# Kernel tuning notes

Measured on AMD Instinct MI355X. Metric: run time of the kernel, lower is better.

Reference implementation:

```python
import jax, jax.numpy as jnp
import numpy as np

N_NODES = 50000
N_EDGES = 800000
QRY = 128
KEY = 128
VAL = 128
HEADS = 8
HEAD_FEATS = VAL // HEADS
BN_EPS = 1e-5


def setup_inputs() -> dict:
    key = jax.random.key(0)
    ks = jax.random.split(key, 12)
    inp = {
        "ft_q": jax.random.normal(ks[0], (N_NODES, QRY), dtype=jnp.float32),
        "ft_k": jax.random.normal(ks[1], (N_NODES, KEY), dtype=jnp.float32),
        "src": jax.random.randint(ks[2], (N_EDGES,), 0, N_NODES, dtype=jnp.int32),
        "dst": jax.random.randint(ks[3], (N_EDGES,), 0, N_NODES, dtype=jnp.int32),
        # learned params
        "Wq": jax.random.normal(ks[4], (VAL, QRY), dtype=jnp.float32) / np.sqrt(QRY),
        "bq": jnp.zeros((VAL,), dtype=jnp.float32),
        "Wk": jax.random.normal(ks[5], (VAL, KEY), dtype=jnp.float32) / np.sqrt(KEY),
        "Wv": jax.random.normal(ks[6], (VAL, QRY), dtype=jnp.float32) / np.sqrt(QRY),
        "attn_e": jax.random.normal(ks[7], (VAL,), dtype=jnp.float32),
        "bn_q_g": jnp.ones((QRY,), dtype=jnp.float32),
        "bn_q_b": jnp.zeros((QRY,), dtype=jnp.float32),
        "bn_k_g": jnp.ones((KEY,), dtype=jnp.float32),
        "bn_k_b": jnp.zeros((KEY,), dtype=jnp.float32),
    }
    return inp


def _batch_norm(x, gamma, beta):
    # training-mode BatchNorm1d: normalize over batch dim
    mean = jnp.mean(x, axis=0, keepdims=True)
    var = jnp.var(x, axis=0, keepdims=True)
    return (x - mean) * jax.lax.rsqrt(var + BN_EPS) * gamma + beta


def reference(ft_q, ft_k, src, dst, Wq, bq, Wk, Wv, attn_e,
              bn_q_g, bn_q_b, bn_k_g, bn_k_b):
    ft_q = _batch_norm(ft_q, bn_q_g, bn_q_b)
    ft_k = _batch_norm(ft_k, bn_k_g, bn_k_b)

    q = ft_q @ Wq.T + bq                      # [N, VAL]
    k = ft_k @ Wk.T                           # [N, VAL]
    v = (ft_q @ Wv.T).reshape(-1, HEADS, HEAD_FEATS)  # [N, H, D]

    # u_add_v: per-edge e = q[src] + k[dst]
    e = q[src] + k[dst]                       # [E, VAL]
    e = (attn_e * jax.nn.sigmoid(e)).reshape(-1, HEADS, HEAD_FEATS).sum(-1)  # [E, H]

    # edge_softmax grouped by destination node
    m = jax.ops.segment_max(e, dst, num_segments=N_NODES)   # [N, H]
    ex = jnp.exp(e - m[dst])                                # [E, H]
    s = jax.ops.segment_sum(ex, dst, num_segments=N_NODES)  # [N, H]
    a = ex / s[dst]                                         # [E, H]

    # u_mul_e_sum: scatter-sum of v[src] * a over destination
    msg = v[src] * a[:, :, None]                            # [E, H, D]
    rst = jax.ops.segment_sum(msg, dst, num_segments=N_NODES)  # [N, H, D]
    return rst.reshape(-1, VAL)
```

## Files before the change

### kernel.cpp

```cpp
#include <hip/hip_runtime.h>

#define N_NODES 50000
#define N_EDGES 800000
#define FEATS 128
#define NCHUNK 196
#define CPAD 50176
#define GEMM_BX 196
#define GEMM_BLOCKS 392
#define SCAT_BLOCKS 3125
#define NTILE 782
#define NF_WAVES 8192
#define STAT_BLOCKS 256
#define HSEG 128
#define ESEG 6250
#define HHALF 25088

typedef __attribute__((ext_vector_type(8))) short bf16x8;
typedef __attribute__((ext_vector_type(4))) float f32x4;
typedef union { uint4 u; bf16x8 v; } pack8;

__device__ __forceinline__ unsigned short f2bf(float f){
  unsigned u = __float_as_uint(f);
  u += 0x7FFF + ((u >> 16) & 1);
  return (unsigned short)(u >> 16);
}
__device__ __forceinline__ unsigned cvtpk(float lo, float hi){
  unsigned r;
  asm("v_cvt_pk_bf16_f32 %0, %1, %2" : "=v"(r) : "v"(lo), "v"(hi));
  return r;
}
__device__ __forceinline__ void unpack8(uint4 p, float* f){
  f[0]=__uint_as_float(p.x << 16); f[1]=__uint_as_float(p.x & 0xffff0000u);
  f[2]=__uint_as_float(p.y << 16); f[3]=__uint_as_float(p.y & 0xffff0000u);
  f[4]=__uint_as_float(p.z << 16); f[5]=__uint_as_float(p.z & 0xffff0000u);
  f[6]=__uint_as_float(p.w << 16); f[7]=__uint_as_float(p.w & 0xffff0000u);
}

__global__ __launch_bounds__(256) void stats_hist_kernel(
    const float* __restrict__ ftq, const float* __restrict__ ftk,
    float* __restrict__ sums, unsigned short* __restrict__ xqb,
    const int* __restrict__ dstE, unsigned short* __restrict__ rankE,
    unsigned short* __restrict__ hmat){
  __shared__ float red[4*FEATS];
  __shared__ unsigned lh[HHALF/2];
  int tid = threadIdx.x, bid = blockIdx.x;
  if (bid < STAT_BLOCKS){
    for (int i = tid; i < 4*FEATS; i += 256) red[i] = 0.f;
    __syncthreads();
    int sub = tid >> 5, c4 = tid & 31;
    const float* Xs = (sub < 4) ? ftq : ftk;
    int so = (sub < 4) ? 0 : 2*FEATS;
    bool isq = (sub < 4);
    float a0=0,a1=0,a2=0,a3=0,b0=0,b1=0,b2=0,b3=0;
    #pragma unroll 4
    for (int r = bid*4 + (sub&3); r < N_NODES; r += STAT_BLOCKS*4){
      float4 x = *(const float4*)(Xs + (size_t)r*FEATS + c4*4);
      if (isq)
        *(uint2*)&xqb[(size_t)r*FEATS + c4*4] = make_uint2(cvtpk(x.x,x.y), cvtpk(x.z,x.w));
      a0+=x.x; b0+=x.x*x.x; a1+=x.y; b1+=x.y*x.y;
      a2+=x.z; b2+=x.z*x.z; a3+=x.w; b3+=x.w*x.w;
    }
    a0 += __shfl_xor(a0,32); a1 += __shfl_xor(a1,32);
    a2 += __shfl_xor(a2,32); a3 += __shfl_xor(a3,32);
    b0 += __shfl_xor(b0,32); b1 += __shfl_xor(b1,32);
    b2 += __shfl_xor(b2,32); b3 += __shfl_xor(b3,32);
    if ((tid & 63) < 32){
      int c0 = c4*4;
      atomicAdd(&red[so + c0+0], a0); atomicAdd(&red[so + c0+1], a1);
      atomicAdd(&red[so + c0+2], a2); atomicAdd(&red[so + c0+3], a3);
      atomicAdd(&red[so + FEATS + c0+0], b0); atomicAdd(&red[so + FEATS + c0+1], b1);
      atomicAdd(&red[so + FEATS + c0+2], b2); atomicAdd(&red[so + FEATS + c0+3], b3);
    }
    __syncthreads();
    for (int i = tid; i < 4*FEATS; i += 256) atomicAdd(&sums[i], red[i]);
  } else {
    int hb = bid - STAT_BLOCKS;
    int seg = hb >> 1, hi = hb & 1;
    int dlo = hi * HHALF;
    for (int i = tid; i < HHALF/2; i += 256) lh[i] = 0;
    __syncthreads();
    int e0 = seg * ESEG;
    for (int t = e0 + tid; t < e0 + ESEG; t += 256){
      int d = dstE[t] - dlo;
      if ((unsigned)d < (unsigned)HHALF){
        unsigned sh = (d & 1) * 16;
        unsigned old = atomicAdd(&lh[d >> 1], 1u << sh);
        rankE[t] = (unsigned short)((old >> sh) & 0xffffu);
      }
    }
    __syncthreads();
    unsigned* row = (unsigned*)(hmat + (size_t)hb * HHALF);
    for (int i = tid; i < HHALF/2; i += 256) row[i] = lh[i];
  }
}

__global__ __launch_bounds__(256) void colscan_fold_kernel(
    const unsigned short* __restrict__ hmat, unsigned short* __restrict__ hbase,
    int* __restrict__ loc, int* __restrict__ csums,
    const float* __restrict__ Wq, const float* __restrict__ bq,
    const float* __restrict__ Wk, const float* __restrict__ Wv,
    const float* __restrict__ gq, const float* __restrict__ bqn,
    const float* __restrict__ gk, const float* __restrict__ bkn,
    const float* __restrict__ sums,
    unsigned short* __restrict__ Wb, float* __restrict__ bias){
  __shared__ int s[256];
  int tid = threadIdx.x, bid = blockIdx.x;
  if (bid < NCHUNK){
    int d = bid*256 + tid;
    int hi = (d >= HHALF) ? 1 : 0;
    int col = d - hi*HHALF;
    const unsigned short* hp = hmat + (size_t)hi*HHALF + col;
    unsigned short* bp = hbase + (size_t)hi*HHALF + col;
    int run = 0;
    #pragma unroll 8
    for (int sg = 0; sg < HSEG; sg++){
      int v = hp[(size_t)sg*2*HHALF];
      bp[(size_t)sg*2*HHALF] = (unsigned short)run;
      run += v;
    }
    s[tid] = run; __syncthreads();
    for (int dd = 1; dd < 256; dd <<= 1){
      int tv = (tid >= dd) ? s[tid-dd] : 0; __syncthreads();
      s[tid] += tv; __syncthreads();
    }
    loc[d] = s[tid] - run;
    if (tid == 255) csums[bid] = s[255];
  } else {
    int wv = (bid - NCHUNK)*4 + (tid >> 6);
    int lane = tid & 63;
    int m = wv >> 7;
    int o = wv & 127;
    const float* Wsrc = (m==0) ? Wq : (m==1) ? Wv : Wk;
    const float* g   = (m==2) ? gk : gq;
    const float* bb  = (m==2) ? bkn : bqn;
    const float* s0  = (m==2) ? (sums + 2*FEATS) : sums;
    const float invN = 1.0f / (float)N_NODES;
    float acc = 0.f;
    unsigned short w2[2];
    int i0 = lane*2;
    #pragma unroll
    for (int t = 0; t < 2; t++){
      int i = i0 + t;
      float mean = s0[i]*invN;
      float var  = s0[FEATS+i]*invN - mean*mean;
      float rstd = rsqrtf(var + 1e-5f);
      float scale = g[i]*rstd;
      float shift = bb[i] - mean*scale;
      float w = Wsrc[o*FEATS + i];
      w2[t] = f2bf(w*scale);
      acc += shift*w;
    }
    ((unsigned*)Wb)[(m*FEATS*FEATS + o*FEATS + i0) >> 1] =
        (unsigned)w2[0] | ((unsigned)w2[1] << 16);
    #pragma unroll
    for (int off = 1; off < 64; off <<= 1) acc += __shfl_xor(acc, off);
    if (lane == 0) bias[m*FEATS + o] = acc + ((m==0) ? bq[o] : 0.f);
  }
}

__global__ __launch_bounds__(256) void bscan_kernel(
    const int* __restrict__ csums, int* __restrict__ bscan){
  __shared__ int s[256];
  int tid = threadIdx.x;
  int v = (tid < NCHUNK) ? csums[tid] : 0;
  s[tid] = v; __syncthreads();
  for (int d = 1; d < 256; d <<= 1){
    int tv = (tid >= d) ? s[tid-d] : 0; __syncthreads();
    s[tid] += tv; __syncthreads();
  }
  if (tid < NCHUNK) bscan[tid] = s[tid] - v;
}

__global__ __launch_bounds__(256) void scatter_kernel(
    const int* __restrict__ dstE, const int* __restrict__ srcE,
    const int* __restrict__ loc, const int* __restrict__ bscan,
    const unsigned short* __restrict__ rankE, const unsigned short* __restrict__ hbase,
    int* __restrict__ src_csr){
  int t = blockIdx.x*256 + threadIdx.x;
  int d = dstE[t];
  int seg = t / ESEG;
  int hi = (d >= HHALF) ? 1 : 0;
  int base = (int)hbase[(size_t)(seg*2 + hi)*HHALF + (d - hi*HHALF)];
  src_csr[loc[d] + bscan[d >> 8] + base + (int)rankE[t]] = srcE[t];
}

__global__ __launch_bounds__(256) void gemm_kernel(
    const unsigned short* __restrict__ xqb, const float* __restrict__ ftk,
    const unsigned short* __restrict__ Wball, const float* __restrict__ biasall,
    unsigned short* __restrict__ qv, unsigned short* __restrict__ kb){
  __shared__ unsigned short Bs[2][FEATS][FEATS];
  int tid = threadIdx.x, bid = blockIdx.x;
  int isk = (bid >= GEMM_BX);
  int bx = isk ? bid - GEMM_BX : bid;
  int nplanes = isk ? 1 : 2;
  {
    for (int p = 0; p < nplanes; p++){
      int m = isk ? 2 : p;
      const uint4* srcp = (const uint4*)(Wball + m*FEATS*FEATS);
      for (int idx = tid; idx < FEATS*FEATS/8; idx += 256){
        int n = idx >> 4, ck = idx & 15;
        *(uint4*)&Bs[p][n][(ck ^ (n & 15))*8] = srcp[idx];
      }
    }
  }
  __syncthreads();
  int wave = tid >> 6, lane = tid & 63;
  int mrow = lane & 15, quad = lane >> 4;
  float bv[2][8];
  #pragma unroll
  for (int p = 0; p < 2; p++)
    #pragma unroll
    for (int ct = 0; ct < 8; ct++)
      bv[p][ct] = biasall[(isk ? 2 : p)*FEATS + ct*16 + mrow];
  uint4 cur[4], nxt[4];
  auto loadA = [&](uint4* buf, int t){
    int arow = t*64 + wave*16 + mrow;
    if (!isk){
      const unsigned short* xp = xqb + (size_t)arow*FEATS + quad*8;
      buf[0] = *(const uint4*)xp;
      buf[1] = *(const uint4*)(xp + 32);
      buf[2] = *(const uint4*)(xp + 64);
      buf[3] = *(const uint4*)(xp + 96);
    } else {
      bool rok = arow < N_NODES;
      const float* xp = ftk + (size_t)(rok ? arow : 0)*FEATS + quad*8;
      #pragma unroll
      for (int kt = 0; kt < 4; kt++){
        float4 x0 = *(const float4*)(xp + kt*32);
        float4 x1 = *(const float4*)(xp + kt*32 + 4);
        if (!rok){ x0 = make_float4(0.f,0.f,0.f,0.f); x1 = x0; }
        buf[kt].x = cvtpk(x0.x, x0.y); buf[kt].y = cvtpk(x0.z, x0.w);
        buf[kt].z = cvtpk(x1.x, x1.y); buf[kt].w = cvtpk(x1.z, x1.w);
      }
    }
  };
  loadA(cur, bx);
  for (int t = bx; t < NTILE; t += GEMM_BX){
    int tn = t + GEMM_BX;
    if (tn < NTILE) loadA(nxt, tn);
    f32x4 acc[2][8];
    #pragma unroll
    for (int p = 0; p < 2; p++)
      #pragma unroll
      for (int i = 0; i < 8; i++) acc[p][i] = (f32x4){0.f,0.f,0.f,0.f};
    #pragma unroll
    for (int kt = 0; kt < 4; kt++){
      pack8 a; a.u = cur[kt];
      #pragma unroll
      for (int ct = 0; ct < 8; ct++){
        bf16x8 b0 = *(bf16x8*)&Bs[0][ct*16 + mrow][((kt*4 + quad) ^ mrow)*8];
        acc[0][ct] = __builtin_amdgcn_mfma_f32_16x16x32_bf16(a.v, b0, acc[0][ct], 0, 0, 0);
      }
      if (!isk){
        #pragma unroll
        for (int ct = 0; ct < 8; ct++){
          bf16x8 b1 = *(bf16x8*)&Bs[1][ct*16 + mrow][((kt*4 + quad) ^ mrow)*8];
          acc[1][ct] = __builtin_amdgcn_mfma_f32_16x16x32_bf16(a.v, b1, acc[1][ct], 0, 0, 0);
        }
      }
    }
    int row0 = t*64;
    #pragma unroll
    for (int p = 0; p < 2; p++){
      if (isk && p) break;
      unsigned short* Out = isk ? kb : (qv + p*128);
      const int ostride = isk ? FEATS : 256;
      #pragma unroll
      for (int ct = 0; ct < 8; ct++){
        int col = ct*16 + mrow;
        #pragma unroll
        for (int v = 0; v < 4; v++){
          int orow = row0 + wave*16 + quad*4 + v;
          float sv = acc[p][ct][v] + bv[p][ct];
          float pf = __shfl_xor(sv, 1);
          if (!(mrow & 1) && orow < N_NODES)
            *(unsigned*)&Out[(size_t)orow*ostride + col] = cvtpk(sv, pf);
        }
      }
    }
    #pragma unroll
    for (int i = 0; i < 4; i++) cur[i] = nxt[i];
  }
}

__global__ __launch_bounds__(256) void node_fused_kernel(
    const unsigned short* __restrict__ qv, const unsigned short* __restrict__ kb,
    const float* __restrict__ attn, const int* __restrict__ src_csr,
    const int* __restrict__ loc, const int* __restrict__ bscan,
    float* __restrict__ out){
  int tid = threadIdx.x;
  int lane = tid & 63;
  int h = lane & 7, g = lane >> 3;
  int w = blockIdx.x*4 + (tid >> 6);
  const float L2E = 1.44269504f;
  float ar[16];
  {
    const uint4* ap = (const uint4*)(attn + h*16);
    uint4 a0 = ap[0], a1 = ap[1], a2 = ap[2], a3 = ap[3];
    ar[0]=__uint_as_float(a0.x); ar[1]=__uint_as_float(a0.y); ar[2]=__uint_as_float(a0.z); ar[3]=__uint_as_float(a0.w);
    ar[4]=__uint_as_float(a1.x); ar[5]=__uint_as_float(a1.y); ar[6]=__uint_as_float(a1.z); ar[7]=__uint_as_float(a1.w);
    ar[8]=__uint_as_float(a2.x); ar[9]=__uint_as_float(a2.y); ar[10]=__uint_as_float(a2.z); ar[11]=__uint_as_float(a2.w);
    ar[12]=__uint_as_float(a3.x); ar[13]=__uint_as_float(a3.y); ar[14]=__uint_as_float(a3.z); ar[15]=__uint_as_float(a3.w);
  }
  for (int n = w; n < N_NODES; n += NF_WAVES){
    int off0 = loc[n]   + bscan[n>>8];
    int off1 = loc[n+1] + bscan[(n+1)>>8];
    int deg = off1 - off0;
    if (deg == 0){
      ((float2*)(out + (size_t)n*FEATS))[lane] = make_float2(0.f, 0.f);
      continue;
    }
    float kf2[16];
    {
      const unsigned short* kr = kb + (size_t)n*FEATS + h*16;
      uint4 k0 = *(const uint4*)kr;
      uint4 k1 = *(const uint4*)(kr + 8);
      float kf[16]; unpack8(k0, kf); unpack8(k1, kf+8);
      #pragma unroll
      for (int i = 0; i < 16; i++) kf2[i] = -L2E * kf[i];
    }
    float ssum = 0.f;
    float acc[16];
    #pragma unroll
    for (int i = 0; i < 16; i++) acc[i] = 0.f;
    if (g < deg){
      int sA = src_csr[off0 + g];
      int jB = g + 8;
      int sB = (jB < deg) ? src_csr[off0 + jB] : sA;
      const unsigned short* pA = qv + (size_t)sA*256 + h*16;
      uint4 qa0 = *(const uint4*)pA;
      uint4 qa1 = *(const uint4*)(pA + 8);
      while (true){
        uint4 va0 = *(const uint4*)(pA + 128);
        uint4 va1 = *(const uint4*)(pA + 136);
        const unsigned short* pB = qv + (size_t)sB*256 + h*16;
        uint4 qb0 = *(const uint4*)pB;
        uint4 qb1 = *(const uint4*)(pB + 8);
        int jC = jB + 8;
        int sC = (jC < deg) ? src_csr[off0 + jC] : sB;
        float qf[16]; unpack8(qa0, qf); unpack8(qa1, qf+8);
        float ta = 0.f, tb = 0.f, tc = 0.f, td = 0.f;
        #pragma unroll
        for (int i = 0; i < 16; i += 4){
          float x0 = fmaf(qf[i+0], -L2E, kf2[i+0]);
          float x1 = fmaf(qf[i+1], -L2E, kf2[i+1]);
          float x2 = fmaf(qf[i+2], -L2E, kf2[i+2]);
          float x3 = fmaf(qf[i+3], -L2E, kf2[i+3]);
          ta = fmaf(ar[i+0], __builtin_amdgcn_rcpf(1.f + __builtin_amdgcn_exp2f(x0)), ta);
          tb = fmaf(ar[i+1], __builtin_amdgcn_rcpf(1.f + __builtin_amdgcn_exp2f(x1)), tb);
          tc = fmaf(ar[i+2], __builtin_amdgcn_rcpf(1.f + __builtin_amdgcn_exp2f(x2)), tc);
          td = fmaf(ar[i+3], __builtin_amdgcn_rcpf(1.f + __builtin_amdgcn_exp2f(x3)), td);
        }
        float t = (ta + tb) + (tc + td);
        float ex = __builtin_amdgcn_exp2f(t * L2E);
        ssum += ex;
        float vf[16]; unpack8(va0, vf); unpack8(va1, vf+8);
        #pragma unroll
        for (int i = 0; i < 16; i++) acc[i] = fmaf(ex, vf[i], acc[i]);
        if (jB >= deg) break;
        qa0 = qb0; qa1 = qb1; pA = pB;
        jB = jC; sB = sC;
      }
    }
    ssum += __shfl_xor(ssum, 8); ssum += __shfl_xor(ssum, 16); ssum += __shfl_xor(ssum, 32);
    #pragma unroll
    for (int i = 0; i < 16; i++){
      acc[i] += __shfl_xor(acc[i], 8);
      acc[i] += __shfl_xor(acc[i], 16);
      acc[i] += __shfl_xor(acc[i], 32);
    }
    if (g == 0){
      float inv_s = 1.f / ssum;
      float4* op = (float4*)(out + (size_t)n*FEATS + h*16);
      op[0] = make_float4(acc[0]*inv_s, acc[1]*inv_s, acc[2]*inv_s, acc[3]*inv_s);
      op[1] = make_float4(acc[4]*inv_s, acc[5]*inv_s, acc[6]*inv_s, acc[7]*inv_s);
      op[2] = make_float4(acc[8]*inv_s, acc[9]*inv_s, acc[10]*inv_s, acc[11]*inv_s);
      op[3] = make_float4(acc[12]*inv_s, acc[13]*inv_s, acc[14]*inv_s, acc[15]*inv_s);
    }
  }
}

extern "C" void kernel_launch(void* const* d_in, const int* in_sizes, int n_in,
                              void* d_out, int out_size, void* d_ws, size_t ws_size,
                              hipStream_t stream){
  (void)in_sizes; (void)n_in; (void)out_size; (void)ws_size;
  const float* ftq  = (const float*)d_in[0];
  const float* ftk  = (const float*)d_in[1];
  const int*   srcE = (const int*)d_in[2];
  const int*   dstE = (const int*)d_in[3];
  const float* Wq   = (const float*)d_in[4];
  const float* bq   = (const float*)d_in[5];
  const float* Wk   = (const float*)d_in[6];
  const float* Wv   = (const float*)d_in[7];
  const float* attn = (const float*)d_in[8];
  const float* gq   = (const float*)d_in[9];
  const float* bqn  = (const float*)d_in[10];
  const float* gk   = (const float*)d_in[11];
  const float* bkn  = (const float*)d_in[12];

  char* ws = (char*)d_ws;
  float* sums    = (float*)(ws + 0);
  int*   csums   = (int*)(ws + 2048);
  int*   bscan   = (int*)(ws + 2848);
  int*   loc     = (int*)(ws + 4096);
  int*   src_csr = (int*)(ws + 204800);
  unsigned short* rankE = (unsigned short*)(ws + 3404800);
  unsigned short* hmat  = (unsigned short*)(ws + 5004800);
  unsigned short* hbase = (unsigned short*)(ws + 17849856);
  unsigned short* Wb    = (unsigned short*)(ws + 30694912);
  float* biasf   = (float*)(ws + 30793216);
  unsigned short* xqb = (unsigned short*)(ws + 30794752);
  unsigned short* qv  = (unsigned short*)(ws + 43639808);
  unsigned short* kb  = (unsigned short*)(ws + 69239808);
  float* out = (float*)d_out;

  hipMemsetAsync(ws, 0, 2048, stream);

  hipLaunchKernelGGL(stats_hist_kernel, dim3(2*STAT_BLOCKS), dim3(256), 0, stream,
                     ftq, ftk, sums, xqb, dstE, rankE, hmat);
  hipLaunchKernelGGL(colscan_fold_kernel, dim3(NCHUNK + 96), dim3(256), 0, stream,
                     hmat, hbase, loc, csums,
                     Wq, bq, Wk, Wv, gq, bqn, gk, bkn, sums, Wb, biasf);
  hipLaunchKernelGGL(bscan_kernel, dim3(1), dim3(256), 0, stream, csums, bscan);
  hipLaunchKernelGGL(scatter_kernel, dim3(SCAT_BLOCKS), dim3(256), 0, stream,
                     dstE, srcE, loc, bscan, rankE, hbase, src_csr);
  hipLaunchKernelGGL(gemm_kernel, dim3(GEMM_BLOCKS), dim3(256), 0, stream,
                     xqb, ftk, Wb, biasf, qv, kb);
  hipLaunchKernelGGL(node_fused_kernel, dim3(NF_WAVES/4), dim3(256), 0, stream,
                     qv, kb, attn, src_csr, loc, bscan, out);
}
```

Baseline: 267.1 us.

## Fold chunk sums into histogram kernel and merge scatter with GEMM launch

Per-chunk destination counts are now computed in the histogram blocks using wave reductions and atomics into csums, so the chunk-offset scan moves into an extra block of the colscan kernel and the single-block bscan launch is removed. The CSR scatter runs as extra blocks of the GEMM kernel, so scatter and GEMM share one launch and can overlap. This cuts two kernel launches and their serialization gaps. In exchange it adds atomics, a larger memset, and scatter blocks that reserve the GEMM kernel's large shared memory allocation, which may lower their occupancy.

```diff
diff --git a/kernel.cpp b/kernel.cpp
--- a/kernel.cpp
+++ b/kernel.cpp
@@ -14,6 +14,7 @@
 #define HSEG 128
 #define ESEG 6250
 #define HHALF 25088
+#define CPH 98
 
 typedef __attribute__((ext_vector_type(8))) short bf16x8;
 typedef __attribute__((ext_vector_type(4))) float f32x4;
@@ -40,7 +41,7 @@
     const float* __restrict__ ftq, const float* __restrict__ ftk,
     float* __restrict__ sums, unsigned short* __restrict__ xqb,
     const int* __restrict__ dstE, unsigned short* __restrict__ rankE,
-    unsigned short* __restrict__ hmat){
+    unsigned short* __restrict__ hmat, int* __restrict__ csums){
   __shared__ float red[4*FEATS];
   __shared__ unsigned lh[HHALF/2];
   int tid = threadIdx.x, bid = blockIdx.x;
@@ -91,12 +92,21 @@
     __syncthreads();
     unsigned* row = (unsigned*)(hmat + (size_t)hb * HHALF);
     for (int i = tid; i < HHALF/2; i += 256) row[i] = lh[i];
+    int wv = tid >> 6, ln = tid & 63;
+    for (int c = wv; c < CPH; c += 4){
+      unsigned w0 = lh[c*128 + ln];
+      unsigned w1 = lh[c*128 + 64 + ln];
+      unsigned t = (w0 & 0xffffu) + (w0 >> 16) + (w1 & 0xffffu) + (w1 >> 16);
+      #pragma unroll
+      for (int o = 1; o < 64; o <<= 1) t += __shfl_xor((int)t, o);
+      if (ln == 0 && t) atomicAdd(&csums[hi*CPH + c], (int)t);
+    }
   }
 }
 
 __global__ __launch_bounds__(256) void colscan_fold_kernel(
     const unsigned short* __restrict__ hmat, unsigned short* __restrict__ hbase,
-    int* __restrict__ loc, int* __restrict__ csums,
+    int* __restrict__ loc, const int* __restrict__ csums, int* __restrict__ bscan,
     const float* __restrict__ Wq, const float* __restrict__ bq,
     const float* __restrict__ Wk, const float* __restrict__ Wv,
     const float* __restrict__ gq, const float* __restrict__ bqn,
@@ -124,7 +134,14 @@
       s[tid] += tv; __syncthreads();
     }
     loc[d] = s[tid] - run;
-    if (tid == 255) csums[bid] = s[255];
+  } else if (bid == NCHUNK + 96){
+    int v = (tid < NCHUNK) ? csums[tid] : 0;
+    s[tid] = v; __syncthreads();
+    for (int dd = 1; dd < 256; dd <<= 1){
+      int tv = (tid >= dd) ? s[tid-dd] : 0; __syncthreads();
+      s[tid] += tv; __syncthreads();
+    }
+    if (tid < NCHUNK) bscan[tid] = s[tid] - v;
   } else {
     int wv = (bid - NCHUNK)*4 + (tid >> 6);
     int lane = tid & 63;
@@ -158,38 +175,25 @@
   }
 }
 
-__global__ __launch_bounds__(256) void bscan_kernel(
-    const int* __restrict__ csums, int* __restrict__ bscan){
-  __shared__ int s[256];
-  int tid = threadIdx.x;
-  int v = (tid < NCHUNK) ? csums[tid] : 0;
-  s[tid] = v; __syncthreads();
-  for (int d = 1; d < 256; d <<= 1){
-    int tv = (tid >= d) ? s[tid-d] : 0; __syncthreads();
-    s[tid] += tv; __syncthreads();
-  }
-  if (tid < NCHUNK) bscan[tid] = s[tid] - v;
-}
-
-__global__ __launch_bounds__(256) void scatter_kernel(
+__global__ __launch_bounds__(256) void gemm_scatter_kernel(
+    const unsigned short* __restrict__ xqb, const float* __restrict__ ftk,
+    const unsigned short* __restrict__ Wball, const float* __restrict__ biasall,
+    unsigned short* __restrict__ qv, unsigned short* __restrict__ kb,
     const int* __restrict__ dstE, const int* __restrict__ srcE,
     const int* __restrict__ loc, const int* __restrict__ bscan,
     const unsigned short* __restrict__ rankE, const unsigned short* __restrict__ hbase,
     int* __restrict__ src_csr){
-  int t = blockIdx.x*256 + threadIdx.x;
-  int d = dstE[t];
-  int seg = t / ESEG;
-  int hi = (d >= HHALF) ? 1 : 0;
-  int base = (int)hbase[(size_t)(seg*2 + hi)*HHALF + (d - hi*HHALF)];
-  src_csr[loc[d] + bscan[d >> 8] + base + (int)rankE[t]] = srcE[t];
-}
-
-__global__ __launch_bounds__(256) void gemm_kernel(
-    const unsigned short* __restrict__ xqb, const float* __restrict__ ftk,
-    const unsigned short* __restrict__ Wball, const float* __restrict__ biasall,
-    unsigned short* __restrict__ qv, unsigned short* __restrict__ kb){
   __shared__ unsigned short Bs[2][FEATS][FEATS];
   int tid = threadIdx.x, bid = blockIdx.x;
+  if (bid >= GEMM_BLOCKS){
+    int t = (bid - GEMM_BLOCKS)*256 + tid;
+    int d = dstE[t];
+    int seg = t / ESEG;
+    int hi = (d >= HHALF) ? 1 : 0;
+    int base = (int)hbase[(size_t)(seg*2 + hi)*HHALF + (d - hi*HHALF)];
+    src_csr[loc[d] + bscan[d >> 8] + base + (int)rankE[t]] = srcE[t];
+    return;
+  }
   int isk = (bid >= GEMM_BX);
   int bx = isk ? bid - GEMM_BX : bid;
   int nplanes = isk ? 1 : 2;
@@ -414,18 +418,15 @@
   unsigned short* kb  = (unsigned short*)(ws + 69239808);
   float* out = (float*)d_out;
 
-  hipMemsetAsync(ws, 0, 2048, stream);
+  hipMemsetAsync(ws, 0, 2832, stream);
 
   hipLaunchKernelGGL(stats_hist_kernel, dim3(2*STAT_BLOCKS), dim3(256), 0, stream,
-                     ftq, ftk, sums, xqb, dstE, rankE, hmat);
-  hipLaunchKernelGGL(colscan_fold_kernel, dim3(NCHUNK + 96), dim3(256), 0, stream,
-                     hmat, hbase, loc, csums,
+                     ftq, ftk, sums, xqb, dstE, rankE, hmat, csums);
+  hipLaunchKernelGGL(colscan_fold_kernel, dim3(NCHUNK + 97), dim3(256), 0, stream,
+                     hmat, hbase, loc, csums, bscan,
                      Wq, bq, Wk, Wv, gq, bqn, gk, bkn, sums, Wb, biasf);
-  hipLaunchKernelGGL(bscan_kernel, dim3(1), dim3(256), 0, stream, csums, bscan);
-  hipLaunchKernelGGL(scatter_kernel, dim3(SCAT_BLOCKS), dim3(256), 0, stream,
-                     dstE, srcE, loc, bscan, rankE, hbase, src_csr);
-  hipLaunchKernelGGL(gemm_kernel, dim3(GEMM_BLOCKS), dim3(256), 0, stream,
-                     xqb, ftk, Wb, biasf, qv, kb);
+  hipLaunchKernelGGL(gemm_scatter_kernel, dim3(GEMM_BLOCKS + SCAT_BLOCKS), dim3(256), 0, stream,
+                     xqb, ftk, Wb, biasf, qv, kb, dstE, srcE, loc, bscan, rankE, hbase, src_csr);
   hipLaunchKernelGGL(node_fused_kernel, dim3(NF_WAVES/4), dim3(256), 0, stream,
                      qv, kb, attn, src_csr, loc, bscan, out);
 }
```

New measurement: 297.4 us. +11.4%, slower.

## Split destination histogram into quarters and fold block scan into colscan kernel

Applied to the files above, without the earlier changes.

The per-segment destination histogram is split into four node quarters instead of two, halving its shared-memory array and doubling the histogram block count. Each histogram block also writes per-256-node chunk totals, so an extra block in the colscan kernel can build the chunk-offset scan, which removes the separate single-block bscan launch. Stats blocks are doubled as well. In exchange, each edge segment's dst array is now read four times instead of twice, and there is an extra wave reduction per histogram block.

```diff
diff --git a/kernel.cpp b/kernel.cpp
--- a/kernel.cpp
+++ b/kernel.cpp
@@ -10,10 +10,12 @@
 #define SCAT_BLOCKS 3125
 #define NTILE 782
 #define NF_WAVES 8192
-#define STAT_BLOCKS 256
+#define STAT_BLOCKS 512
+#define HIST_BLOCKS 512
 #define HSEG 128
 #define ESEG 6250
-#define HHALF 25088
+#define HQ 12544
+#define CPQ 49
 
 typedef __attribute__((ext_vector_type(8))) short bf16x8;
 typedef __attribute__((ext_vector_type(4))) float f32x4;
@@ -40,9 +42,9 @@
     const float* __restrict__ ftq, const float* __restrict__ ftk,
     float* __restrict__ sums, unsigned short* __restrict__ xqb,
     const int* __restrict__ dstE, unsigned short* __restrict__ rankE,
-    unsigned short* __restrict__ hmat){
+    unsigned short* __restrict__ hmat, unsigned short* __restrict__ ctot){
   __shared__ float red[4*FEATS];
-  __shared__ unsigned lh[HHALF/2];
+  __shared__ unsigned lh[HQ/2];
   int tid = threadIdx.x, bid = blockIdx.x;
   if (bid < STAT_BLOCKS){
     for (int i = tid; i < 4*FEATS; i += 256) red[i] = 0.f;
@@ -75,28 +77,37 @@
     for (int i = tid; i < 4*FEATS; i += 256) atomicAdd(&sums[i], red[i]);
   } else {
     int hb = bid - STAT_BLOCKS;
-    int seg = hb >> 1, hi = hb & 1;
-    int dlo = hi * HHALF;
-    for (int i = tid; i < HHALF/2; i += 256) lh[i] = 0;
+    int seg = hb >> 2, q = hb & 3;
+    int dlo = q * HQ;
+    for (int i = tid; i < HQ/2; i += 256) lh[i] = 0;
     __syncthreads();
     int e0 = seg * ESEG;
     for (int t = e0 + tid; t < e0 + ESEG; t += 256){
       int d = dstE[t] - dlo;
-      if ((unsigned)d < (unsigned)HHALF){
+      if ((unsigned)d < (unsigned)HQ){
         unsigned sh = (d & 1) * 16;
         unsigned old = atomicAdd(&lh[d >> 1], 1u << sh);
         rankE[t] = (unsigned short)((old >> sh) & 0xffffu);
       }
     }
     __syncthreads();
-    unsigned* row = (unsigned*)(hmat + (size_t)hb * HHALF);
-    for (int i = tid; i < HHALF/2; i += 256) row[i] = lh[i];
+    unsigned* row = (unsigned*)(hmat + (size_t)hb * HQ);
+    for (int i = tid; i < HQ/2; i += 256) row[i] = lh[i];
+    int wv = tid >> 6, ln = tid & 63;
+    for (int c = wv; c < CPQ; c += 4){
+      unsigned w0 = lh[c*128 + ln];
+      unsigned w1 = lh[c*128 + 64 + ln];
+      unsigned t = (w0 & 0xffffu) + (w0 >> 16) + (w1 & 0xffffu) + (w1 >> 16);
+      #pragma unroll
+      for (int o = 1; o < 64; o <<= 1) t += __shfl_xor((int)t, o);
+      if (ln == 0) ctot[hb*CPQ + c] = (unsigned short)t;
+    }
   }
 }
 
 __global__ __launch_bounds__(256) void colscan_fold_kernel(
     const unsigned short* __restrict__ hmat, unsigned short* __restrict__ hbase,
-    int* __restrict__ loc, int* __restrict__ csums,
+    int* __restrict__ loc, const unsigned short* __restrict__ ctot, int* __restrict__ bscan,
     const float* __restrict__ Wq, const float* __restrict__ bq,
     const float* __restrict__ Wk, const float* __restrict__ Wv,
     const float* __restrict__ gq, const float* __restrict__ bqn,
@@ -106,16 +117,16 @@
   __shared__ int s[256];
   int tid = threadIdx.x, bid = blockIdx.x;
   if (bid < NCHUNK){
+    int q = bid / CPQ;
     int d = bid*256 + tid;
-    int hi = (d >= HHALF) ? 1 : 0;
-    int col = d - hi*HHALF;
-    const unsigned short* hp = hmat + (size_t)hi*HHALF + col;
-    unsigned short* bp = hbase + (size_t)hi*HHALF + col;
+    int col = d - q*HQ;
+    const unsigned short* hp = hmat + (size_t)q*HQ + col;
+    unsigned short* bp = hbase + (size_t)q*HQ + col;
     int run = 0;
     #pragma unroll 8
     for (int sg = 0; sg < HSEG; sg++){
-      int v = hp[(size_t)sg*2*HHALF];
-      bp[(size_t)sg*2*HHALF] = (unsigned short)run;
+      int v = hp[(size_t)sg*4*HQ];
+      bp[(size_t)sg*4*HQ] = (unsigned short)run;
       run += v;
     }
     s[tid] = run; __syncthreads();
@@ -124,7 +135,20 @@
       s[tid] += tv; __syncthreads();
     }
     loc[d] = s[tid] - run;
-    if (tid == 255) csums[bid] = s[255];
+  } else if (bid == NCHUNK + 96){
+    int v = 0;
+    if (tid < NCHUNK){
+      int q = tid / CPQ, cc = tid - q*CPQ;
+      const unsigned short* cp = ctot + q*CPQ + cc;
+      #pragma unroll 8
+      for (int sg = 0; sg < HSEG; sg++) v += cp[(size_t)sg*4*CPQ];
+    }
+    s[tid] = v; __syncthreads();
+    for (int dd = 1; dd < 256; dd <<= 1){
+      int tv = (tid >= dd) ? s[tid-dd] : 0; __syncthreads();
+      s[tid] += tv; __syncthreads();
+    }
+    if (tid < NCHUNK) bscan[tid] = s[tid] - v;
   } else {
     int wv = (bid - NCHUNK)*4 + (tid >> 6);
     int lane = tid & 63;
@@ -158,19 +182,6 @@
   }
 }
 
-__global__ __launch_bounds__(256) void bscan_kernel(
-    const int* __restrict__ csums, int* __restrict__ bscan){
-  __shared__ int s[256];
-  int tid = threadIdx.x;
-  int v = (tid < NCHUNK) ? csums[tid] : 0;
-  s[tid] = v; __syncthreads();
-  for (int d = 1; d < 256; d <<= 1){
-    int tv = (tid >= d) ? s[tid-d] : 0; __syncthreads();
-    s[tid] += tv; __syncthreads();
-  }
-  if (tid < NCHUNK) bscan[tid] = s[tid] - v;
-}
-
 __global__ __launch_bounds__(256) void scatter_kernel(
     const int* __restrict__ dstE, const int* __restrict__ srcE,
     const int* __restrict__ loc, const int* __restrict__ bscan,
@@ -179,8 +190,8 @@
   int t = blockIdx.x*256 + threadIdx.x;
   int d = dstE[t];
   int seg = t / ESEG;
-  int hi = (d >= HHALF) ? 1 : 0;
-  int base = (int)hbase[(size_t)(seg*2 + hi)*HHALF + (d - hi*HHALF)];
+  int q = d / HQ;
+  int base = (int)hbase[(size_t)(seg*4 + q)*HQ + (d - q*HQ)];
   src_csr[loc[d] + bscan[d >> 8] + base + (int)rankE[t]] = srcE[t];
 }
 
@@ -400,28 +411,27 @@
 
   char* ws = (char*)d_ws;
   float* sums    = (float*)(ws + 0);
-  int*   csums   = (int*)(ws + 2048);
-  int*   bscan   = (int*)(ws + 2848);
+  int*   bscan   = (int*)(ws + 2048);
   int*   loc     = (int*)(ws + 4096);
   int*   src_csr = (int*)(ws + 204800);
   unsigned short* rankE = (unsigned short*)(ws + 3404800);
   unsigned short* hmat  = (unsigned short*)(ws + 5004800);
   unsigned short* hbase = (unsigned short*)(ws + 17849856);
-  unsigned short* Wb    = (unsigned short*)(ws + 30694912);
-  float* biasf   = (float*)(ws + 30793216);
-  unsigned short* xqb = (unsigned short*)(ws + 30794752);
-  unsigned short* qv  = (unsigned short*)(ws + 43639808);
-  unsigned short* kb  = (unsigned short*)(ws + 69239808);
+  unsigned short* ctot  = (unsigned short*)(ws + 30694912);
+  unsigned short* Wb    = (unsigned short*)(ws + 30745088);
+  float* biasf   = (float*)(ws + 30843392);
+  unsigned short* xqb = (unsigned short*)(ws + 30844928);
+  unsigned short* qv  = (unsigned short*)(ws + 43689984);
+  unsigned short* kb  = (unsigned short*)(ws + 69289984);
   float* out = (float*)d_out;
 
   hipMemsetAsync(ws, 0, 2048, stream);
 
-  hipLaunchKernelGGL(stats_hist_kernel, dim3(2*STAT_BLOCKS), dim3(256), 0, stream,
-                     ftq, ftk, sums, xqb, dstE, rankE, hmat);
-  hipLaunchKernelGGL(colscan_fold_kernel, dim3(NCHUNK + 96), dim3(256), 0, stream,
-                     hmat, hbase, loc, csums,
+  hipLaunchKernelGGL(stats_hist_kernel, dim3(STAT_BLOCKS + HIST_BLOCKS), dim3(256), 0, stream,
+                     ftq, ftk, sums, xqb, dstE, rankE, hmat, ctot);
+  hipLaunchKernelGGL(colscan_fold_kernel, dim3(NCHUNK + 97), dim3(256), 0, stream,
+                     hmat, hbase, loc, ctot, bscan,
                      Wq, bq, Wk, Wv, gq, bqn, gk, bkn, sums, Wb, biasf);
-  hipLaunchKernelGGL(bscan_kernel, dim3(1), dim3(256), 0, stream, csums, bscan);
   hipLaunchKernelGGL(scatter_kernel, dim3(SCAT_BLOCKS), dim3(256), 0, stream,
                      dstE, srcE, loc, bscan, rankE, hbase, src_csr);
   hipLaunchKernelGGL(gemm_kernel, dim3(GEMM_BLOCKS), dim3(256), 0, stream,
```

Result: faster. 259.5 us (-2.9%).
